# Performance work log

Hardware: AMD Instinct MI355X
Metric: run time of the kernel (lower is better)

Reference implementation:

```python
import jax, jax.numpy as jnp
import numpy as np

HEADS = 8
B, N, DIM = 8, 1024, 128  # n must be a perfect square (H=W=32)
LN_EPS = 1e-5


def _region_means(xg):
    """Four-quadrant region means per position via integral image.
    xg: [b,H,W,d] -> [b,H,W,4,d]. For position (h,w) the torch code pools:
      r1 = x[:, :h+1, :w+1], r2 = x[:, :h+1, w:], r3 = x[:, h:, :w+1], r4 = x[:, h:, w:]
    """
    b, H, W, d = xg.shape
    # padded 2D prefix sum: P[:, i, j] = sum over rows<i, cols<j
    P = jnp.pad(jnp.cumsum(jnp.cumsum(xg, axis=1), axis=2),
                ((0, 0), (1, 0), (1, 0), (0, 0)))
    r1 = P[:, 1:, 1:]                                              # sum x[:h+1,:w+1]
    r2 = P[:, 1:, -1:] - P[:, 1:, :-1]                             # sum x[:h+1, w:]
    r3 = P[:, -1:, 1:] - P[:, :-1, 1:]                             # sum x[h:, :w+1]
    r4 = P[:, -1:, -1:] - P[:, :-1, -1:] - P[:, -1:, :-1] + P[:, :-1, :-1]
    ah = jnp.arange(H, dtype=xg.dtype)
    aw = jnp.arange(W, dtype=xg.dtype)
    hp1 = (ah + 1.0)[:, None]   # h+1
    wp1 = (aw + 1.0)[None, :]   # w+1
    hr = (H - ah)[:, None]      # H-h
    wr = (W - aw)[None, :]      # W-w
    c1 = (hp1 * wp1)[None, :, :, None]
    c2 = (hp1 * wr)[None, :, :, None]
    c3 = (hr * wp1)[None, :, :, None]
    c4 = (hr * wr)[None, :, :, None]
    return jnp.stack([r1 / c1, r2 / c2, r3 / c3, r4 / c4], axis=3)


def setup_inputs() -> dict:
    key = jax.random.key(0)
    ks = jax.random.split(key, 10)
    s = 0.02
    return {
        "x": jax.random.normal(ks[0], (B, N, DIM), jnp.float32),
        "ln_g": jnp.ones((DIM,), jnp.float32),
        "ln_b": jnp.zeros((DIM,), jnp.float32),
        "Wqkv": jax.random.normal(ks[1], (DIM, 3 * HEADS * DIM), jnp.float32) * s,
        "bqkv": jax.random.normal(ks[2], (3 * HEADS * DIM,), jnp.float32) * s,
        "Wq": jax.random.normal(ks[3], (DIM, DIM), jnp.float32) * s,
        "Wk": jax.random.normal(ks[4], (DIM, DIM), jnp.float32) * s,
        "Wv": jax.random.normal(ks[5], (DIM, DIM), jnp.float32) * s,
        "Wo": jax.random.normal(ks[6], (DIM, DIM), jnp.float32) * s,
        "bo": jax.random.normal(ks[7], (DIM,), jnp.float32) * s,
        "Wout": jax.random.normal(ks[8], (HEADS * DIM, DIM), jnp.float32) * s,
        "bout": jax.random.normal(ks[9], (DIM,), jnp.float32) * s,
    }


def reference(x, ln_g, ln_b, Wqkv, bqkv, Wq, Wk, Wv, Wo, bo, Wout, bout):
    b, n, dim = x.shape
    H = W = int(n ** 0.5)
    # LayerNorm
    mu = jnp.mean(x, axis=-1, keepdims=True)
    var = jnp.mean(jnp.square(x - mu), axis=-1, keepdims=True)
    xn = (x - mu) * jax.lax.rsqrt(var + LN_EPS) * ln_g + ln_b
    # qkv projection; only q is actually used downstream (k,v chunks are dead)
    qkv = xn @ Wqkv + bqkv
    q = qkv[..., : HEADS * dim].reshape(b, n, HEADS, dim).transpose(0, 2, 1, 3)  # [b,h,n,d]
    # region features, identical across heads -> keep unbroadcast [b,n,4,d]
    regions = _region_means(xn.reshape(b, H, W, dim)).reshape(b, n, 4, dim)
    # RegionAggregator
    qh = q @ Wq                                   # [b,h,n,d]
    k = jnp.einsum('bnrd,de->bnre', regions, Wk)  # [b,n,4,d]
    v = jnp.einsum('bnrd,de->bnre', regions, Wv)
    scale = (dim // HEADS) ** -0.5
    attn = jax.nn.softmax(jnp.einsum('bhnd,bnrd->bhnr', qh, k) * scale, axis=-1)
    agg = jnp.einsum('bhnr,bnrd->bhnd', attn, v)
    out = agg @ Wo + bo                           # [b,h,n,d]
    out = out.transpose(0, 2, 1, 3).reshape(b, n, HEADS * dim)
    return out @ Wout + bout
```

## Files before the change

### kernel.cpp

```cpp
#include <hip/hip_runtime.h>
#include <hip/hip_bf16.h>
#include <stdint.h>

#define HEADS 8
#define NN 1024
#define DIM 128
#define HW 32
#define LN_EPS 1e-5f

typedef __hip_bfloat16 bf16;
typedef __bf16 bf16x8 __attribute__((ext_vector_type(8)));
typedef float floatx4 __attribute__((ext_vector_type(4)));

__device__ __forceinline__ float b2f(bf16 v){ return __bfloat162float(v); }
__device__ __forceinline__ bf16 f2b(float v){ return __float2bfloat16(v); }

__device__ __forceinline__ float ldin(const void* p, size_t i, int f){
    return f ? ((const float*)p)[i] : b2f(((const bf16*)p)[i]);
}
__device__ __forceinline__ float4 ldin4(const void* p, size_t i, int f){
    if (f) return *reinterpret_cast<const float4*>((const float*)p + i);
    ushort4 u = *reinterpret_cast<const ushort4*>((const bf16*)p + i);
    float4 r;
    r.x = b2f(*(bf16*)&u.x); r.y = b2f(*(bf16*)&u.y);
    r.z = b2f(*(bf16*)&u.z); r.w = b2f(*(bf16*)&u.w);
    return r;
}
__device__ __forceinline__ int dtf(const void* g){
    return (((const uint32_t*)g)[0] == 0x3F800000u) ? 1 : 0;
}

__global__ __launch_bounds__(256) void lnscan_kernel(const void* __restrict__ x,
                                                     const void* __restrict__ g,
                                                     const void* __restrict__ bta,
                                                     bf16* __restrict__ xn,
                                                     float* __restrict__ P){
    __shared__ float lnv[32][128];
    int f = dtf(g);
    int b = blockIdx.x >> 5, hh = blockIdx.x & 31;
    int wv = threadIdx.x >> 6, lane = threadIdx.x & 63;
    float gl0 = ldin(g, lane, f),    gl1 = ldin(g, lane+64, f);
    float bl0 = ldin(bta, lane, f),  bl1 = ldin(bta, lane+64, f);
    size_t rowbase = (size_t)b*NN + (size_t)hh*HW;
#pragma unroll
    for (int rnd=0; rnd<8; rnd++){
        int w = rnd*4 + wv;
        size_t base = (rowbase + w)*DIM;
        float v0 = ldin(x, base+lane,    f);
        float v1 = ldin(x, base+lane+64, f);
        float s = v0+v1, ss = v0*v0+v1*v1;
        for (int o=32;o;o>>=1){ s += __shfl_xor(s,o,64); ss += __shfl_xor(ss,o,64); }
        float mu = s * (1.0f/DIM);
        float var = ss * (1.0f/DIM) - mu*mu;
        float rs = rsqrtf(var + LN_EPS);
        float y0 = (v0-mu)*rs*gl0 + bl0;
        float y1 = (v1-mu)*rs*gl1 + bl1;
        xn[base+lane]    = f2b(y0);
        xn[base+lane+64] = f2b(y1);
        lnv[w][lane]    = y0;
        lnv[w][lane+64] = y1;
    }
    __syncthreads();
    if (threadIdx.x < 128){
        int c = threadIdx.x;
        float run = 0.f;
        float* Pr = P + rowbase*DIM + c;
#pragma unroll
        for (int w=0; w<HW; w++){
            run += lnv[w][c];
            Pr[(size_t)w*DIM] = run;
        }
    }
}

__global__ __launch_bounds__(128) void colscan_kernel(float* __restrict__ P){
    int b = blockIdx.x >> 5, w = blockIdx.x & 31, c = threadIdx.x;
    float* Pc = P + ((size_t)(b*NN + w))*DIM + c;
    float run = 0.f;
    for (int h=0; h<HW; h++){
        size_t o = (size_t)h*HW*DIM;
        run += Pc[o]; Pc[o] = run;
    }
}

__global__ __launch_bounds__(256) void prep_kernel(const void* __restrict__ Wqkv,
                                                   const void* __restrict__ bqkv,
                                                   const void* __restrict__ Wq,
                                                   const void* __restrict__ Wk,
                                                   const void* __restrict__ Wv,
                                                   const void* __restrict__ Wo,
                                                   const void* __restrict__ bo,
                                                   const void* __restrict__ Wout,
                                                   const void* __restrict__ ln_g,
                                                   bf16* __restrict__ WhT,
                                                   bf16* __restrict__ WhoT,
                                                   bf16* __restrict__ WkvT,
                                                   float* __restrict__ bq,
                                                   float* __restrict__ bfin_part){
    __shared__ float S1[128][132];
    __shared__ float S2[8][132];
    int f = dtf(ln_g);
    int t = threadIdx.x;
    int blk = blockIdx.x;
    if (blk < 128){
        int h = blk >> 4, dc = blk & 15;
#pragma unroll
        for (int i=0;i<16;i++){
            int idx4 = (t + i*256)*4;
            int k = idx4 >> 7, e = idx4 & 127;
            *reinterpret_cast<float4*>(&S1[k][e]) = ldin4(Wq, idx4, f);
        }
        {
            int idx4 = t*4;
            int dl = idx4 >> 7, k = idx4 & 127;
            *reinterpret_cast<float4*>(&S2[dl][k]) =
                ldin4(Wqkv, (size_t)(dc*8+dl)*3072 + h*128 + k, f);
        }
        __syncthreads();
        int d = t & 7;
        int e0 = (t >> 3) * 4;
        float acc[4] = {0.f,0.f,0.f,0.f};
        for (int k=0;k<128;k++){
            float a = S2[d][k];
            float4 wv = *reinterpret_cast<const float4*>(&S1[k][e0]);
            acc[0] += a*wv.x; acc[1] += a*wv.y; acc[2] += a*wv.z; acc[3] += a*wv.w;
        }
#pragma unroll
        for (int i=0;i<4;i++)
            WhT[(size_t)(h*128 + e0 + i)*128 + dc*8 + d] = f2b(acc[i]);
    } else if (blk < 256){
        int h = (blk-128) >> 4, dc = (blk-128) & 15;
#pragma unroll
        for (int i=0;i<16;i++){
            int idx4 = (t + i*256)*4;
            int k = idx4 >> 7, e = idx4 & 127;
            *reinterpret_cast<float4*>(&S1[k][e]) =
                ldin4(Wout, (size_t)(h*128 + k)*128 + e, f);
        }
        {
            int idx4 = t*4;
            int dl = idx4 >> 7, k = idx4 & 127;
            *reinterpret_cast<float4*>(&S2[dl][k]) =
                ldin4(Wo, (size_t)(dc*8+dl)*128 + k, f);
        }
        __syncthreads();
        int d = t & 7;
        int e0 = (t >> 3) * 4;
        float acc[4] = {0.f,0.f,0.f,0.f};
        for (int k=0;k<128;k++){
            float a = S2[d][k];
            float4 wv = *reinterpret_cast<const float4*>(&S1[k][e0]);
            acc[0] += a*wv.x; acc[1] += a*wv.y; acc[2] += a*wv.z; acc[3] += a*wv.w;
        }
#pragma unroll
        for (int i=0;i<4;i++)
            WhoT[(size_t)(e0 + i)*1024 + h*128 + dc*8 + d] = f2b(acc[i]);
    } else {
        int sub = blk - 256;
        if (sub < 8){
            int h = sub;
            int e = t & 127, kh = t >> 7;
            float s = 0.f;
            for (int k=kh*64; k<kh*64+64; k++)
                s += ldin(bqkv, h*128 + k, f) * ldin(Wq, (size_t)k*128 + e, f);
            S1[kh][e] = s;
            __syncthreads();
            if (t < 128) bq[h*128 + t] = S1[0][t] + S1[1][t];
        } else if (sub < 16){
            int h = sub - 8;
            if (t < 128) S2[0][t] = ldin(bo, t, f);
            __syncthreads();
            int e = t & 127, half = t >> 7;
            float s = 0.f;
            for (int k = half*64; k < half*64 + 64; k++)
                s += S2[0][k] * ldin(Wout, (size_t)(h*128 + k)*128 + e, f);
            S1[half][e] = s;
            __syncthreads();
            if (t < 128) bfin_part[h*128 + t] = S1[0][t] + S1[1][t];
        } else {
            const void* W = (sub == 16) ? Wk : Wv;
            int base = (sub == 16) ? 0 : 128;
#pragma unroll
            for (int i=0;i<16;i++){
                int idx4 = (t + i*256)*4;
                int d = idx4 >> 7, e = idx4 & 127;
                *reinterpret_cast<float4*>(&S1[d][e]) = ldin4(W, idx4, f);
            }
            __syncthreads();
            for (int i=0;i<64;i++){
                int idx = t + i*256; int e = idx >> 7, d = idx & 127;
                WkvT[(size_t)(base + e)*128 + d] = f2b(S1[d][e]);
            }
        }
    }
}

__global__ __launch_bounds__(256) void attn_fused_kernel(const float* __restrict__ P,
                                                         const bf16* __restrict__ WkvT,
                                                         const bf16* __restrict__ WhT,
                                                         const bf16* __restrict__ WhoT,
                                                         const float* __restrict__ bq,
                                                         const float* __restrict__ bfin_part,
                                                         const void* __restrict__ bout,
                                                         const bf16* __restrict__ xn,
                                                         const void* __restrict__ ln_g,
                                                         void* __restrict__ out){
    __shared__ __align__(16) char pool[59136];
    bf16 (*As)[136]     = reinterpret_cast<bf16(*)[136]>(pool);
    bf16 (*kS)[16][136] = reinterpret_cast<bf16(*)[16][136]>(pool);
    bf16 (*Bs)[136]     = reinterpret_cast<bf16(*)[136]>(pool + 17408);
    bf16 (*qL)[16][136] = reinterpret_cast<bf16(*)[16][136]>(pool + 17408);
    bf16 (*vS)[16][136] = reinterpret_cast<bf16(*)[16][136]>(pool + 34816);
    bf16 (*xnS)[136]    = reinterpret_cast<bf16(*)[136]>(pool + 52224);
    float* logits       = reinterpret_cast<float*>(pool + 56576);
    float4* probsS      = reinterpret_cast<float4*>(pool + 57088);

    int f = dtf(ln_g);
    int t = threadIdx.x;
    int bn0 = blockIdx.x * 16;
    {
        int bn_local = t >> 4;
        int c0 = (t & 15) * 8;
        int bn = bn0 + bn_local;
        int b = bn >> 10, n = bn & 1023;
        int hh = n >> 5, ww = n & 31;
        const float* Pb = P + (size_t)b*NN*DIM;
        auto ld8 = [&](int h, int w, float* o){
            if (h==0 || w==0){
#pragma unroll
                for (int j=0;j<8;j++) o[j] = 0.f;
                return;
            }
            const float* p = Pb + ((size_t)((h-1)*HW + (w-1)))*DIM + c0;
            float4 u = *reinterpret_cast<const float4*>(p);
            float4 v = *reinterpret_cast<const float4*>(p+4);
            o[0]=u.x;o[1]=u.y;o[2]=u.z;o[3]=u.w;o[4]=v.x;o[5]=v.y;o[6]=v.z;o[7]=v.w;
        };
        float f_h1 = (float)(hh+1), f_w1 = (float)(ww+1);
        float f_hr = (float)(HW-hh), f_wr = (float)(HW-ww);
        float a0[8], a1[8];
        ld8(hh+1, ww+1, a0);
#pragma unroll
        for (int j=0;j<8;j++) As[bn_local*4 + 0][c0+j] = f2b(a0[j] / (f_h1*f_w1));
        ld8(hh+1, HW, a0); ld8(hh+1, ww, a1);
#pragma unroll
        for (int j=0;j<8;j++) As[bn_local*4 + 1][c0+j] = f2b((a0[j]-a1[j]) / (f_h1*f_wr));
        ld8(HW, ww+1, a0); ld8(hh, ww+1, a1);
#pragma unroll
        for (int j=0;j<8;j++) As[bn_local*4 + 2][c0+j] = f2b((a0[j]-a1[j]) / (f_hr*f_w1));
        float a2[8], a3[8];
        ld8(HW, HW, a0); ld8(hh, HW, a1); ld8(HW, ww, a2); ld8(hh, ww, a3);
#pragma unroll
        for (int j=0;j<8;j++)
            As[bn_local*4 + 3][c0+j] = f2b((a0[j]-a1[j]-a2[j]+a3[j]) / (f_hr*f_wr));
        *reinterpret_cast<uint4*>(&xnS[t >> 4][(t & 15)*8]) =
            *reinterpret_cast<const uint4*>(&xn[(size_t)(bn0 + (t >> 4))*DIM + (t & 15)*8]);
    }
    int w = t >> 6, lane = t & 63;
    int r = lane & 15, q = lane >> 4;
    floatx4 acc[16];
#pragma unroll
    for (int i=0;i<16;i++) acc[i] = (floatx4){0.f,0.f,0.f,0.f};
    for (int half=0; half<2; half++){
        __syncthreads();
#pragma unroll
        for (int i=0;i<8;i++){
            int id = t + i*256;
            int row = id >> 4, c8 = id & 15;
            *reinterpret_cast<uint4*>(&Bs[row][c8*8]) =
                *reinterpret_cast<const uint4*>(&WkvT[(size_t)(half*128 + row)*128 + c8*8]);
        }
        __syncthreads();
#pragma unroll
        for (int kc=0;kc<4;kc++){
            bf16x8 a = *reinterpret_cast<const bf16x8*>(&As[w*16 + r][kc*32 + q*8]);
#pragma unroll
            for (int nt=0;nt<8;nt++){
                bf16x8 b = *reinterpret_cast<const bf16x8*>(&Bs[nt*16 + r][kc*32 + q*8]);
                acc[half*8+nt] = __builtin_amdgcn_mfma_f32_16x16x32_bf16(a, b, acc[half*8+nt], 0, 0, 0);
            }
        }
    }
    __syncthreads();
#pragma unroll
    for (int nt=0;nt<8;nt++){
#pragma unroll
        for (int i=0;i<4;i++){
            int rowg = w*16 + q*4 + i;
            kS[rowg & 3][rowg >> 2][nt*16 + r] = f2b(acc[nt][i]);
            vS[rowg & 3][rowg >> 2][nt*16 + r] = f2b(acc[8+nt][i]);
        }
    }
    __syncthreads();
    bf16x8 kf[4];
#pragma unroll
    for (int kc=0;kc<4;kc++)
        kf[kc] = *reinterpret_cast<const bf16x8*>(&kS[w][r][kc*32 + q*8]);
    for (int g=0; g<2; g++){
        floatx4 qa[4][2];
#pragma unroll
        for (int hh=0;hh<4;hh++){ qa[hh][0]=(floatx4){0,0,0,0}; qa[hh][1]=(floatx4){0,0,0,0}; }
#pragma unroll
        for (int kc=0;kc<4;kc++){
            bf16x8 a = *reinterpret_cast<const bf16x8*>(&xnS[r][kc*32 + q*8]);
#pragma unroll
            for (int hh=0;hh<4;hh++){
                int h = g*4 + hh;
#pragma unroll
                for (int nl=0;nl<2;nl++){
                    int e = (w*2 + nl)*16 + r;
                    bf16x8 b = *reinterpret_cast<const bf16x8*>(
                        &WhT[((size_t)(h*128 + e))*128 + kc*32 + q*8]);
                    qa[hh][nl] = __builtin_amdgcn_mfma_f32_16x16x32_bf16(a, b, qa[hh][nl], 0, 0, 0);
                }
            }
        }
        __syncthreads();
#pragma unroll
        for (int hh=0;hh<4;hh++){
            int h = g*4 + hh;
#pragma unroll
            for (int nl=0;nl<2;nl++){
                int col = (w*2 + nl)*16 + r;
                float bb = bq[h*128 + col];
#pragma unroll
                for (int i=0;i<4;i++)
                    qL[hh][q*4 + i][col] = f2b(qa[hh][nl][i] + bb);
            }
        }
        __syncthreads();
#pragma unroll
        for (int hh=0;hh<4;hh++){
            floatx4 s = (floatx4){0.f,0.f,0.f,0.f};
#pragma unroll
            for (int kc=0;kc<4;kc++){
                bf16x8 a = *reinterpret_cast<const bf16x8*>(&qL[hh][r][kc*32 + q*8]);
                s = __builtin_amdgcn_mfma_f32_16x16x32_bf16(a, kf[kc], s, 0, 0, 0);
            }
            if ((r >> 2) == q){
                int i = r & 3;
                float d = (i==0)?s[0]:(i==1)?s[1]:(i==2)?s[2]:s[3];
                logits[(r*8 + g*4 + hh)*4 + w] = d;
            }
        }
    }
    __syncthreads();
    if (t < 128){
        int bn = t >> 3, h = t & 7;
        const float* L = &logits[(bn*8 + h)*4];
        float l0 = L[0]*0.25f, l1 = L[1]*0.25f, l2 = L[2]*0.25f, l3 = L[3]*0.25f;
        float m = fmaxf(fmaxf(l0,l1),fmaxf(l2,l3));
        float e0 = __expf(l0-m), e1=__expf(l1-m), e2=__expf(l2-m), e3=__expf(l3-m);
        float inv = 1.0f/(e0+e1+e2+e3);
        probsS[bn*8 + h] = (float4){e0*inv, e1*inv, e2*inv, e3*inv};
    }
    __syncthreads();
    float4 pv[8];
#pragma unroll
    for (int h=0;h<8;h++) pv[h] = probsS[r*8 + h];
    floatx4 oacc[2];
    oacc[0] = (floatx4){0.f,0.f,0.f,0.f};
    oacc[1] = (floatx4){0.f,0.f,0.f,0.f};
#pragma unroll
    for (int kc=0;kc<4;kc++){
        int c = kc*32 + q*8;
        bf16x8 v0 = *reinterpret_cast<const bf16x8*>(&vS[0][r][c]);
        bf16x8 v1 = *reinterpret_cast<const bf16x8*>(&vS[1][r][c]);
        bf16x8 v2 = *reinterpret_cast<const bf16x8*>(&vS[2][r][c]);
        bf16x8 v3 = *reinterpret_cast<const bf16x8*>(&vS[3][r][c]);
#pragma unroll
        for (int h=0; h<8; h++){
            bf16x8 a;
#pragma unroll
            for (int j=0;j<8;j++){
                float s = pv[h].x*(float)v0[j] + pv[h].y*(float)v1[j]
                        + pv[h].z*(float)v2[j] + pv[h].w*(float)v3[j];
                a[j] = (__bf16)s;
            }
#pragma unroll
            for (int nl=0;nl<2;nl++){
                int e = (w*2 + nl)*16 + r;
                bf16x8 b = *reinterpret_cast<const bf16x8*>(
                    &WhoT[(size_t)e*1024 + h*128 + kc*32 + q*8]);
                oacc[nl] = __builtin_amdgcn_mfma_f32_16x16x32_bf16(a, b, oacc[nl], 0, 0, 0);
            }
        }
    }
#pragma unroll
    for (int nl=0;nl<2;nl++){
        int col = (w*2 + nl)*16 + r;
        float bias = ldin(bout, col, f);
#pragma unroll
        for (int h=0;h<8;h++) bias += bfin_part[h*128 + col];
#pragma unroll
        for (int i=0;i<4;i++){
            int row = bn0 + q*4 + i;
            float v = oacc[nl][i] + bias;
            if (f) ((float*)out)[(size_t)row*DIM + col] = v;
            else   ((bf16*)out)[(size_t)row*DIM + col] = f2b(v);
        }
    }
}

extern "C" void kernel_launch(void* const* d_in, const int* in_sizes, int n_in,
                              void* d_out, int out_size, void* d_ws, size_t ws_size,
                              hipStream_t stream){
    const void* x    = d_in[0];
    const void* ln_g = d_in[1];
    const void* ln_b = d_in[2];
    const void* Wqkv = d_in[3];
    const void* bqkv = d_in[4];
    const void* Wq   = d_in[5];
    const void* Wk   = d_in[6];
    const void* Wv   = d_in[7];
    const void* Wo   = d_in[8];
    const void* bo   = d_in[9];
    const void* Wout = d_in[10];
    const void* bout = d_in[11];

    char* ws = (char*)d_ws;
    size_t off = 0;
    auto alloc = [&](size_t bytes)->char*{
        char* p = ws + off; off += (bytes + 255) & ~size_t(255); return p;
    };
    bf16*  WhT   = (bf16*)alloc((size_t)1024*128*2);
    bf16*  WkvT  = (bf16*)alloc((size_t)256*128*2);
    bf16*  WhoT  = (bf16*)alloc((size_t)128*1024*2);
    float* bq    = (float*)alloc(1024*4);
    float* bfin_part = (float*)alloc(8*128*4);
    float* P     = (float*)alloc((size_t)8*NN*DIM*4);
    bf16*  xn    = (bf16*)alloc((size_t)8192*128*2);

    prep_kernel<<<274, 256, 0, stream>>>(Wqkv, bqkv, Wq, Wk, Wv, Wo, bo, Wout,
                                         ln_g, WhT, WhoT, WkvT, bq, bfin_part);
    lnscan_kernel<<<256, 256, 0, stream>>>(x, ln_g, ln_b, xn, P);
    colscan_kernel<<<256, 128, 0, stream>>>(P);
    attn_fused_kernel<<<512, 256, 0, stream>>>(P, WkvT, WhT, WhoT, bq, bfin_part,
                                               bout, xn, ln_g, d_out);
}
```

Before: 147.3 us.

## Double threads per block in LN-scan and fused attention kernels, re-split MFMA work

The LayerNorm/scan kernel now runs 1024 threads per block, with each wave handling 2 rows instead of 8. The fused attention kernel goes from 4 to 8 waves per block, and the K/V, Q, logits and output MFMA work is split so each wave does a smaller share. K/V weights are read straight from global memory instead of being staged through shared memory. Probabilities move to a padded transposed layout to avoid bank conflicts. The aim is more latency hiding and parallelism per block, at the cost of more barriers, more global weight reads per wave, and possible register limits from launch_bounds(512,4).

```diff
diff --git a/kernel.cpp b/kernel.cpp
--- a/kernel.cpp
+++ b/kernel.cpp
@@ -30,11 +30,11 @@
     return (((const uint32_t*)g)[0] == 0x3F800000u) ? 1 : 0;
 }
 
-__global__ __launch_bounds__(256) void lnscan_kernel(const void* __restrict__ x,
-                                                     const void* __restrict__ g,
-                                                     const void* __restrict__ bta,
-                                                     bf16* __restrict__ xn,
-                                                     float* __restrict__ P){
+__global__ __launch_bounds__(1024) void lnscan_kernel(const void* __restrict__ x,
+                                                      const void* __restrict__ g,
+                                                      const void* __restrict__ bta,
+                                                      bf16* __restrict__ xn,
+                                                      float* __restrict__ P){
     __shared__ float lnv[32][128];
     int f = dtf(g);
     int b = blockIdx.x >> 5, hh = blockIdx.x & 31;
@@ -43,8 +43,8 @@
     float bl0 = ldin(bta, lane, f),  bl1 = ldin(bta, lane+64, f);
     size_t rowbase = (size_t)b*NN + (size_t)hh*HW;
 #pragma unroll
-    for (int rnd=0; rnd<8; rnd++){
-        int w = rnd*4 + wv;
+    for (int rnd=0; rnd<2; rnd++){
+        int w = rnd*16 + wv;
         size_t base = (rowbase + w)*DIM;
         float v0 = ldin(x, base+lane,    f);
         float v1 = ldin(x, base+lane+64, f);
@@ -195,152 +195,153 @@
     }
 }
 
-__global__ __launch_bounds__(256) void attn_fused_kernel(const float* __restrict__ P,
-                                                         const bf16* __restrict__ WkvT,
-                                                         const bf16* __restrict__ WhT,
-                                                         const bf16* __restrict__ WhoT,
-                                                         const float* __restrict__ bq,
-                                                         const float* __restrict__ bfin_part,
-                                                         const void* __restrict__ bout,
-                                                         const bf16* __restrict__ xn,
-                                                         const void* __restrict__ ln_g,
-                                                         void* __restrict__ out){
-    __shared__ __align__(16) char pool[59136];
+__global__ __launch_bounds__(512, 4) void attn_fused_kernel(const float* __restrict__ P,
+                                                            const bf16* __restrict__ WkvT,
+                                                            const bf16* __restrict__ WhT,
+                                                            const bf16* __restrict__ WhoT,
+                                                            const float* __restrict__ bq,
+                                                            const float* __restrict__ bfin_part,
+                                                            const void* __restrict__ bout,
+                                                            const bf16* __restrict__ xn,
+                                                            const void* __restrict__ ln_g,
+                                                            void* __restrict__ out){
+    __shared__ __align__(16) char pool[60800];
     bf16 (*As)[136]     = reinterpret_cast<bf16(*)[136]>(pool);
-    bf16 (*kS)[16][136] = reinterpret_cast<bf16(*)[16][136]>(pool);
-    bf16 (*Bs)[136]     = reinterpret_cast<bf16(*)[136]>(pool + 17408);
-    bf16 (*qL)[16][136] = reinterpret_cast<bf16(*)[16][136]>(pool + 17408);
-    bf16 (*vS)[16][136] = reinterpret_cast<bf16(*)[16][136]>(pool + 34816);
+    bf16 (*vS)[16][136] = reinterpret_cast<bf16(*)[16][136]>(pool);
+    bf16 (*kS)[16][136] = reinterpret_cast<bf16(*)[16][136]>(pool + 17408);
+    bf16 (*qL)[16][136] = reinterpret_cast<bf16(*)[16][136]>(pool + 34816);
     bf16 (*xnS)[136]    = reinterpret_cast<bf16(*)[136]>(pool + 52224);
     float* logits       = reinterpret_cast<float*>(pool + 56576);
-    float4* probsS      = reinterpret_cast<float4*>(pool + 57088);
+    float* pp           = reinterpret_cast<float*>(pool + 58624);
 
     int f = dtf(ln_g);
     int t = threadIdx.x;
     int bn0 = blockIdx.x * 16;
     {
-        int bn_local = t >> 4;
-        int c0 = (t & 15) * 8;
+        int bn_local = t >> 5;
+        int c0 = (t & 31) * 4;
         int bn = bn0 + bn_local;
         int b = bn >> 10, n = bn & 1023;
         int hh = n >> 5, ww = n & 31;
         const float* Pb = P + (size_t)b*NN*DIM;
-        auto ld8 = [&](int h, int w, float* o){
-            if (h==0 || w==0){
-#pragma unroll
-                for (int j=0;j<8;j++) o[j] = 0.f;
-                return;
-            }
+        auto ld4 = [&](int h, int w, float* o){
+            if (h==0 || w==0){ o[0]=o[1]=o[2]=o[3]=0.f; return; }
             const float* p = Pb + ((size_t)((h-1)*HW + (w-1)))*DIM + c0;
             float4 u = *reinterpret_cast<const float4*>(p);
-            float4 v = *reinterpret_cast<const float4*>(p+4);
-            o[0]=u.x;o[1]=u.y;o[2]=u.z;o[3]=u.w;o[4]=v.x;o[5]=v.y;o[6]=v.z;o[7]=v.w;
+            o[0]=u.x;o[1]=u.y;o[2]=u.z;o[3]=u.w;
         };
         float f_h1 = (float)(hh+1), f_w1 = (float)(ww+1);
         float f_hr = (float)(HW-hh), f_wr = (float)(HW-ww);
-        float a0[8], a1[8];
-        ld8(hh+1, ww+1, a0);
-#pragma unroll
-        for (int j=0;j<8;j++) As[bn_local*4 + 0][c0+j] = f2b(a0[j] / (f_h1*f_w1));
-        ld8(hh+1, HW, a0); ld8(hh+1, ww, a1);
-#pragma unroll
-        for (int j=0;j<8;j++) As[bn_local*4 + 1][c0+j] = f2b((a0[j]-a1[j]) / (f_h1*f_wr));
-        ld8(HW, ww+1, a0); ld8(hh, ww+1, a1);
-#pragma unroll
-        for (int j=0;j<8;j++) As[bn_local*4 + 2][c0+j] = f2b((a0[j]-a1[j]) / (f_hr*f_w1));
-        float a2[8], a3[8];
-        ld8(HW, HW, a0); ld8(hh, HW, a1); ld8(HW, ww, a2); ld8(hh, ww, a3);
-#pragma unroll
-        for (int j=0;j<8;j++)
+        float a0[4], a1[4], a2[4], a3[4];
+        ld4(hh+1, ww+1, a0);
+#pragma unroll
+        for (int j=0;j<4;j++) As[bn_local*4 + 0][c0+j] = f2b(a0[j] / (f_h1*f_w1));
+        ld4(hh+1, HW, a0); ld4(hh+1, ww, a1);
+#pragma unroll
+        for (int j=0;j<4;j++) As[bn_local*4 + 1][c0+j] = f2b((a0[j]-a1[j]) / (f_h1*f_wr));
+        ld4(HW, ww+1, a0); ld4(hh, ww+1, a1);
+#pragma unroll
+        for (int j=0;j<4;j++) As[bn_local*4 + 2][c0+j] = f2b((a0[j]-a1[j]) / (f_hr*f_w1));
+        ld4(HW, HW, a0); ld4(hh, HW, a1); ld4(HW, ww, a2); ld4(hh, ww, a3);
+#pragma unroll
+        for (int j=0;j<4;j++)
             As[bn_local*4 + 3][c0+j] = f2b((a0[j]-a1[j]-a2[j]+a3[j]) / (f_hr*f_wr));
-        *reinterpret_cast<uint4*>(&xnS[t >> 4][(t & 15)*8]) =
-            *reinterpret_cast<const uint4*>(&xn[(size_t)(bn0 + (t >> 4))*DIM + (t & 15)*8]);
+        *reinterpret_cast<uint2*>(&xnS[bn_local][c0]) =
+            *reinterpret_cast<const uint2*>(&xn[(size_t)(bn0 + bn_local)*DIM + c0]);
     }
     int w = t >> 6, lane = t & 63;
     int r = lane & 15, q = lane >> 4;
-    floatx4 acc[16];
-#pragma unroll
-    for (int i=0;i<16;i++) acc[i] = (floatx4){0.f,0.f,0.f,0.f};
-    for (int half=0; half<2; half++){
-        __syncthreads();
-#pragma unroll
-        for (int i=0;i<8;i++){
-            int id = t + i*256;
-            int row = id >> 4, c8 = id & 15;
-            *reinterpret_cast<uint4*>(&Bs[row][c8*8]) =
-                *reinterpret_cast<const uint4*>(&WkvT[(size_t)(half*128 + row)*128 + c8*8]);
-        }
-        __syncthreads();
-#pragma unroll
-        for (int kc=0;kc<4;kc++){
-            bf16x8 a = *reinterpret_cast<const bf16x8*>(&As[w*16 + r][kc*32 + q*8]);
-#pragma unroll
-            for (int nt=0;nt<8;nt++){
-                bf16x8 b = *reinterpret_cast<const bf16x8*>(&Bs[nt*16 + r][kc*32 + q*8]);
-                acc[half*8+nt] = __builtin_amdgcn_mfma_f32_16x16x32_bf16(a, b, acc[half*8+nt], 0, 0, 0);
-            }
-        }
-    }
+    int mh = w & 3, nh = w >> 2;
     __syncthreads();
-#pragma unroll
-    for (int nt=0;nt<8;nt++){
+    floatx4 acc[4];
+#pragma unroll
+    for (int i=0;i<4;i++) acc[i] = (floatx4){0.f,0.f,0.f,0.f};
+#pragma unroll
+    for (int kc=0;kc<4;kc++){
+        bf16x8 a = *reinterpret_cast<const bf16x8*>(&As[mh*16 + r][kc*32 + q*8]);
+#pragma unroll
+        for (int nt=0;nt<4;nt++){
+            bf16x8 b = *reinterpret_cast<const bf16x8*>(
+                &WkvT[(size_t)(nh*64 + nt*16 + r)*128 + kc*32 + q*8]);
+            acc[nt] = __builtin_amdgcn_mfma_f32_16x16x32_bf16(a, b, acc[nt], 0, 0, 0);
+        }
+    }
+#pragma unroll
+    for (int nt=0;nt<4;nt++)
 #pragma unroll
         for (int i=0;i<4;i++){
-            int rowg = w*16 + q*4 + i;
-            kS[rowg & 3][rowg >> 2][nt*16 + r] = f2b(acc[nt][i]);
-            vS[rowg & 3][rowg >> 2][nt*16 + r] = f2b(acc[8+nt][i]);
+            int rowg = mh*16 + q*4 + i;
+            kS[rowg & 3][rowg >> 2][nh*64 + nt*16 + r] = f2b(acc[nt][i]);
+        }
+#pragma unroll
+    for (int i=0;i<4;i++) acc[i] = (floatx4){0.f,0.f,0.f,0.f};
+#pragma unroll
+    for (int kc=0;kc<4;kc++){
+        bf16x8 a = *reinterpret_cast<const bf16x8*>(&As[mh*16 + r][kc*32 + q*8]);
+#pragma unroll
+        for (int nt=0;nt<4;nt++){
+            bf16x8 b = *reinterpret_cast<const bf16x8*>(
+                &WkvT[(size_t)(128 + nh*64 + nt*16 + r)*128 + kc*32 + q*8]);
+            acc[nt] = __builtin_amdgcn_mfma_f32_16x16x32_bf16(a, b, acc[nt], 0, 0, 0);
         }
     }
     __syncthreads();
-    bf16x8 kf[4];
-#pragma unroll
-    for (int kc=0;kc<4;kc++)
-        kf[kc] = *reinterpret_cast<const bf16x8*>(&kS[w][r][kc*32 + q*8]);
+#pragma unroll
+    for (int nt=0;nt<4;nt++)
+#pragma unroll
+        for (int i=0;i<4;i++){
+            int rowg = mh*16 + q*4 + i;
+            vS[rowg & 3][rowg >> 2][nh*64 + nt*16 + r] = f2b(acc[nt][i]);
+        }
+    int rgA = w >> 2, rgB = rgA + 2;
+    int hl = w & 3;
+    bf16x8 kfA[4], kfB[4];
+#pragma unroll
+    for (int kc=0;kc<4;kc++){
+        kfA[kc] = *reinterpret_cast<const bf16x8*>(&kS[rgA][r][kc*32 + q*8]);
+        kfB[kc] = *reinterpret_cast<const bf16x8*>(&kS[rgB][r][kc*32 + q*8]);
+    }
+    int hq = w >> 1, nl = w & 1;
     for (int g=0; g<2; g++){
-        floatx4 qa[4][2];
-#pragma unroll
-        for (int hh=0;hh<4;hh++){ qa[hh][0]=(floatx4){0,0,0,0}; qa[hh][1]=(floatx4){0,0,0,0}; }
+        floatx4 qa[4];
+#pragma unroll
+        for (int i=0;i<4;i++) qa[i] = (floatx4){0.f,0.f,0.f,0.f};
 #pragma unroll
         for (int kc=0;kc<4;kc++){
             bf16x8 a = *reinterpret_cast<const bf16x8*>(&xnS[r][kc*32 + q*8]);
 #pragma unroll
-            for (int hh=0;hh<4;hh++){
-                int h = g*4 + hh;
-#pragma unroll
-                for (int nl=0;nl<2;nl++){
-                    int e = (w*2 + nl)*16 + r;
-                    bf16x8 b = *reinterpret_cast<const bf16x8*>(
-                        &WhT[((size_t)(h*128 + e))*128 + kc*32 + q*8]);
-                    qa[hh][nl] = __builtin_amdgcn_mfma_f32_16x16x32_bf16(a, b, qa[hh][nl], 0, 0, 0);
-                }
+            for (int nt=0;nt<4;nt++){
+                int e = nl*64 + nt*16 + r;
+                bf16x8 b = *reinterpret_cast<const bf16x8*>(
+                    &WhT[((size_t)((g*4 + hq)*128 + e))*128 + kc*32 + q*8]);
+                qa[nt] = __builtin_amdgcn_mfma_f32_16x16x32_bf16(a, b, qa[nt], 0, 0, 0);
             }
         }
         __syncthreads();
 #pragma unroll
-        for (int hh=0;hh<4;hh++){
-            int h = g*4 + hh;
-#pragma unroll
-            for (int nl=0;nl<2;nl++){
-                int col = (w*2 + nl)*16 + r;
-                float bb = bq[h*128 + col];
-#pragma unroll
-                for (int i=0;i<4;i++)
-                    qL[hh][q*4 + i][col] = f2b(qa[hh][nl][i] + bb);
-            }
+        for (int nt=0;nt<4;nt++){
+            int col = nl*64 + nt*16 + r;
+            float bb = bq[(g*4 + hq)*128 + col];
+#pragma unroll
+            for (int i=0;i<4;i++)
+                qL[hq][q*4 + i][col] = f2b(qa[nt][i] + bb);
         }
         __syncthreads();
-#pragma unroll
-        for (int hh=0;hh<4;hh++){
-            floatx4 s = (floatx4){0.f,0.f,0.f,0.f};
+        {
+            floatx4 sA = (floatx4){0.f,0.f,0.f,0.f};
+            floatx4 sB = (floatx4){0.f,0.f,0.f,0.f};
 #pragma unroll
             for (int kc=0;kc<4;kc++){
-                bf16x8 a = *reinterpret_cast<const bf16x8*>(&qL[hh][r][kc*32 + q*8]);
-                s = __builtin_amdgcn_mfma_f32_16x16x32_bf16(a, kf[kc], s, 0, 0, 0);
+                bf16x8 a = *reinterpret_cast<const bf16x8*>(&qL[hl][r][kc*32 + q*8]);
+                sA = __builtin_amdgcn_mfma_f32_16x16x32_bf16(a, kfA[kc], sA, 0, 0, 0);
+                sB = __builtin_amdgcn_mfma_f32_16x16x32_bf16(a, kfB[kc], sB, 0, 0, 0);
             }
             if ((r >> 2) == q){
                 int i = r & 3;
-                float d = (i==0)?s[0]:(i==1)?s[1]:(i==2)?s[2]:s[3];
-                logits[(r*8 + g*4 + hh)*4 + w] = d;
+                float dA = (i==0)?sA[0]:(i==1)?sA[1]:(i==2)?sA[2]:sA[3];
+                float dB = (i==0)?sB[0]:(i==1)?sB[1]:(i==2)?sB[2]:sB[3];
+                logits[(r*8 + g*4 + hl)*4 + rgA] = dA;
+                logits[(r*8 + g*4 + hl)*4 + rgB] = dB;
             }
         }
     }
@@ -352,15 +353,21 @@
         float m = fmaxf(fmaxf(l0,l1),fmaxf(l2,l3));
         float e0 = __expf(l0-m), e1=__expf(l1-m), e2=__expf(l2-m), e3=__expf(l3-m);
         float inv = 1.0f/(e0+e1+e2+e3);
-        probsS[bn*8 + h] = (float4){e0*inv, e1*inv, e2*inv, e3*inv};
+        pp[0*136 + h*17 + bn] = e0*inv;
+        pp[1*136 + h*17 + bn] = e1*inv;
+        pp[2*136 + h*17 + bn] = e2*inv;
+        pp[3*136 + h*17 + bn] = e3*inv;
     }
     __syncthreads();
     float4 pv[8];
 #pragma unroll
-    for (int h=0;h<8;h++) pv[h] = probsS[r*8 + h];
-    floatx4 oacc[2];
-    oacc[0] = (floatx4){0.f,0.f,0.f,0.f};
-    oacc[1] = (floatx4){0.f,0.f,0.f,0.f};
+    for (int h=0;h<8;h++){
+        pv[h].x = pp[0*136 + h*17 + r];
+        pv[h].y = pp[1*136 + h*17 + r];
+        pv[h].z = pp[2*136 + h*17 + r];
+        pv[h].w = pp[3*136 + h*17 + r];
+    }
+    floatx4 oacc = (floatx4){0.f,0.f,0.f,0.f};
 #pragma unroll
     for (int kc=0;kc<4;kc++){
         int c = kc*32 + q*8;
@@ -377,25 +384,20 @@
                         + pv[h].z*(float)v2[j] + pv[h].w*(float)v3[j];
                 a[j] = (__bf16)s;
             }
-#pragma unroll
-            for (int nl=0;nl<2;nl++){
-                int e = (w*2 + nl)*16 + r;
-                bf16x8 b = *reinterpret_cast<const bf16x8*>(
-                    &WhoT[(size_t)e*1024 + h*128 + kc*32 + q*8]);
-                oacc[nl] = __builtin_amdgcn_mfma_f32_16x16x32_bf16(a, b, oacc[nl], 0, 0, 0);
-            }
-        }
-    }
-#pragma unroll
-    for (int nl=0;nl<2;nl++){
-        int col = (w*2 + nl)*16 + r;
+            bf16x8 b = *reinterpret_cast<const bf16x8*>(
+                &WhoT[(size_t)(w*16 + r)*1024 + h*128 + kc*32 + q*8]);
+            oacc = __builtin_amdgcn_mfma_f32_16x16x32_bf16(a, b, oacc, 0, 0, 0);
+        }
+    }
+    {
+        int col = w*16 + r;
         float bias = ldin(bout, col, f);
 #pragma unroll
         for (int h=0;h<8;h++) bias += bfin_part[h*128 + col];
 #pragma unroll
         for (int i=0;i<4;i++){
             int row = bn0 + q*4 + i;
-            float v = oacc[nl][i] + bias;
+            float v = oacc[i] + bias;
             if (f) ((float*)out)[(size_t)row*DIM + col] = v;
             else   ((bf16*)out)[(size_t)row*DIM + col] = f2b(v);
         }
@@ -433,8 +435,8 @@
 
     prep_kernel<<<274, 256, 0, stream>>>(Wqkv, bqkv, Wq, Wk, Wv, Wo, bo, Wout,
                                          ln_g, WhT, WhoT, WkvT, bq, bfin_part);
-    lnscan_kernel<<<256, 256, 0, stream>>>(x, ln_g, ln_b, xn, P);
+    lnscan_kernel<<<256, 1024, 0, stream>>>(x, ln_g, ln_b, xn, P);
     colscan_kernel<<<256, 128, 0, stream>>>(P);
-    attn_fused_kernel<<<512, 256, 0, stream>>>(P, WkvT, WhT, WhoT, bq, bfin_part,
+    attn_fused_kernel<<<512, 512, 0, stream>>>(P, WkvT, WhT, WhoT, bq, bfin_part,
                                                bout, xn, ln_g, d_out);
 }
```

Result: no change. 145.2 us (-1.4%).
